# Performance work log

Hardware: AMD Instinct MI355X
Metric: run time of the kernel (lower is better)

Reference implementation:

```python
import jax, jax.numpy as jnp
import numpy as np

B, N, OBS, ACT = 128, 32, 64, 16
D = OBS + ACT       # obs_z_input_dim = 80
H = 64              # hardcoded hidden width
WOUT = 64           # weight_output_dim (d_k_weight)
ZOUT = 64           # obs_z_output_dim (d_k_obsz)
FIN = OBS + ZOUT    # final_input_dim = 128
FOUT = 1            # final_output_dim


def _lin_params(key, fan_in, fan_out):
    k1, k2 = jax.random.split(key)
    w = jax.random.normal(k1, (fan_in, fan_out), jnp.float32) / np.sqrt(fan_in).astype(np.float32)
    b = jax.random.normal(k2, (fan_out,), jnp.float32) * 0.01
    return w, b


def setup_inputs() -> dict:
    key = jax.random.key(0)
    ks = jax.random.split(key, 16)
    inp = {
        "states": jax.random.normal(ks[0], (B, N, OBS), jnp.float32),
        "policies": jax.random.uniform(ks[1], (B, N, ACT), jnp.float32),
        "actions": jax.random.uniform(ks[2], (B, N, ACT), jnp.float32),
    }
    specs = [("kw", OBS, WOUT), ("qw", OBS, WOUT), ("ko", D, ZOUT),
             ("qo", D, ZOUT), ("av", D, ZOUT), ("fv", FIN, FOUT)]
    for idx, (nm, din, dout) in enumerate(specs):
        w1, b1 = _lin_params(ks[3 + 2 * idx], din, H)
        w2, b2 = _lin_params(ks[4 + 2 * idx], H, dout)
        inp[nm + "1_w"], inp[nm + "1_b"] = w1, b1
        inp[nm + "2_w"], inp[nm + "2_b"] = w2, b2
    return inp


def _mlp(x, w1, b1, w2, b2):
    return jax.nn.leaky_relu(x @ w1 + b1) @ w2 + b2


def reference(states, policies, actions,
              kw1_w, kw1_b, kw2_w, kw2_b,
              qw1_w, qw1_b, qw2_w, qw2_b,
              ko1_w, ko1_b, ko2_w, ko2_b,
              qo1_w, qo1_b, qo2_w, qo2_b,
              av1_w, av1_b, av2_w, av2_b,
              fv1_w, fv1_b, fv2_w, fv2_b):
    # --- mixing weight between taken actions and policies ---
    key_z = _mlp(states, kw1_w, kw1_b, kw2_w, kw2_b)    # [B,N,WOUT]
    query_z = _mlp(states, qw1_w, qw1_b, qw2_w, qw2_b)  # [B,N,WOUT]
    # torch: bmm(q, k^T).transpose(1,2) => weight_z[b,a,j] = sigmoid(q[b,j].k[b,a]/sqrt(dk))
    scores_z = jnp.einsum('bad,bjd->baj', key_z, query_z)
    weight_z = jax.nn.sigmoid(scores_z / np.float32(np.sqrt(WOUT)))[..., None]  # [B,N,N,1]

    # z[b,a,j] = w[b,a,j]*actions[b,j] + (1-w)*policies[b,j]
    z = weight_z * actions[:, None, :, :] + (1.0 - weight_z) * policies[:, None, :, :]  # [B,N,N,ACT]
    states_b = jnp.broadcast_to(states[:, None, :, :], (B, N, N, OBS))  # states_rep[b,a,j]=states[b,j]
    obs_z = jnp.concatenate([states_b, z], axis=-1)                     # [B,N,N,D]

    # source_obsz one-hot-diag trick selects obs_z[b,a,a] (broadcast over j)
    diag = jnp.arange(N)
    source = obs_z[:, diag, diag, :]                                    # [B,N,D]
    key_obsz = _mlp(source, ko1_w, ko1_b, ko2_w, ko2_b)                 # [B,N,ZOUT]
    query_obsz = _mlp(obs_z, qo1_w, qo1_b, qo2_w, qo2_b)                # [B,N,N,ZOUT]
    scores_obsz = jnp.sum(key_obsz[:, :, None, :] * query_obsz, axis=-1)  # [B,N,N]
    weight_obsz = jax.nn.softmax(scores_obsz / np.float32(np.sqrt(ZOUT)), axis=-1)
    ret_weight_obsz = weight_obsz[..., None]                            # [B,N,N,1]

    # obs_z_pi[b,a,k,j] = cat(states[b,j], policies[b,j]) if j==k else obs_z[b,a,j]
    # (place_zs / place_policies masking). The attention-value MLP is pointwise
    # over the last dim, so apply it to the two distinct branches and combine:
    vals = _mlp(obs_z, av1_w, av1_b, av2_w, av2_b)                      # [B,N,N,ZOUT]
    sp = jnp.concatenate([states, policies], axis=-1)                   # [B,N,D]
    vals_pi = _mlp(sp, av1_w, av1_b, av2_w, av2_b)                      # [B,N,ZOUT]

    w = weight_obsz  # broadcast weight w5[b,a,k,j] = w[b,a,j]
    sum_all = jnp.einsum('baj,bajd->bad', w, vals)                      # [B,N,ZOUT]
    node_features = (sum_all[:, :, None, :]
                     - w[..., None] * vals
                     + w[..., None] * vals_pi[:, None, :, :]) / N       # [B,N,N,ZOUT]

    node_in = jnp.concatenate([states_b, node_features], axis=-1)       # [B,N,N,FIN]
    value = _mlp(node_in, fv1_w, fv1_b, fv2_w, fv2_b)                   # [B,N,N,1]
    return value, weight_z, ret_weight_obsz
```

## Files before the change

kernel.cpp:

```cpp
#include <hip/hip_runtime.h>

#define NN   32
#define HID  64

typedef __attribute__((ext_vector_type(8))) short bf16x8;
typedef __attribute__((ext_vector_type(4))) float f32x4;
typedef unsigned short u16;
typedef unsigned int   u32;

__device__ __forceinline__ float leaky(float v) { return v >= 0.f ? v : 0.01f * v; }
__device__ __forceinline__ float wsum64(float p) {
#pragma unroll
    for (int o = 32; o; o >>= 1) p += __shfl_xor(p, o);
    return p;
}
__device__ __forceinline__ u16 f2bf(float f) {
    union { float f; u32 u; } v; v.f = f;
    return (u16)((v.u + 0x7FFFu + ((v.u >> 16) & 1)) >> 16);
}
__device__ __forceinline__ bf16x8 pack8(const float* v) {
    bf16x8 r;
#pragma unroll
    for (int e = 0; e < 8; ++e) r[e] = (short)f2bf(v[e]);
    return r;
}
__device__ __forceinline__ int swz(int row, int col)   { return row * 64 + ((((col >> 3) ^ (row & 7)) << 3) | (col & 7)); }
__device__ __forceinline__ int swz32(int row, int col) { return row * 32 + ((((col >> 3) ^ (row & 3)) << 3) | (col & 7)); }

__device__ __forceinline__ f32x4 gemm64(f32x4 C, const u16* A, const u16* W, int lm, int kb8, int bcol) {
#pragma unroll
    for (int k0 = 0; k0 < 64; k0 += 32) {
        const int g = (k0 >> 3) + kb8;
        const bf16x8 a = *(const bf16x8*)&A[lm * 64 + ((g ^ (lm & 7)) << 3)];
        const bf16x8 w = *(const bf16x8*)&W[bcol * 64 + ((g ^ (bcol & 7)) << 3)];
        C = __builtin_amdgcn_mfma_f32_16x16x32_bf16(a, w, C, 0, 0, 0);
    }
    return C;
}
__device__ __forceinline__ f32x4 gemm32(f32x4 C, const u16* A, const u16* W, int lm, int kb8, int bcol) {
    const bf16x8 a = *(const bf16x8*)&A[lm * 32 + ((kb8 ^ (lm & 3)) << 3)];
    const bf16x8 w = *(const bf16x8*)&W[bcol * 32 + ((kb8 ^ (bcol & 3)) << 3)];
    return __builtin_amdgcn_mfma_f32_16x16x32_bf16(a, w, C, 0, 0, 0);
}

#define W_KW1  0
#define W_KW2  4096
#define W_QW1  8192
#define W_QW2  12288
#define W_KO1A 16384
#define W_KO2  20480
#define W_QO2  24576
#define W_QO1A 28672
#define W_AV1A 32768
#define W_FV1A 36864
#define W_KO1B 40960
#define W_QO1B 43008
#define W_AV1B 45056

__global__ __launch_bounds__(256)
void prep_kernel(const float* __restrict__ av2_w, const float* __restrict__ av2_b,
                 const float* __restrict__ fv1_w,
                 const float* __restrict__ kw1_w, const float* __restrict__ kw2_w,
                 const float* __restrict__ qw1_w, const float* __restrict__ qw2_w,
                 const float* __restrict__ ko1_w, const float* __restrict__ ko2_w,
                 const float* __restrict__ qo2_w, const float* __restrict__ qo1_w,
                 const float* __restrict__ av1_w,
                 u16* __restrict__ MT, float* __restrict__ c, u16* __restrict__ wt)
{
    const int blk = blockIdx.x, t = threadIdx.x;
    if (blk == 0) {
        const int h = t & 63, jg = t >> 6;
        __shared__ float sA[4096];
        for (int i = t; i < 4096; i += 256) sA[i] = av2_w[i];
        __syncthreads();
        const float* W = fv1_w + 4096;
        float acc[16];
#pragma unroll
        for (int i = 0; i < 16; ++i) acc[i] = 0.f;
        for (int m = 0; m < 64; ++m) {
            const float w = W[m * 64 + h];
#pragma unroll
            for (int i = 0; i < 16; ++i)
                acc[i] = fmaf(sA[(jg + 4 * i) * 64 + m], w, acc[i]);
        }
#pragma unroll
        for (int i = 0; i < 16; ++i) { const int k = jg + 4 * i; MT[swz(h, k)] = f2bf(acc[i]); }
        if (t < 64) {
            float s = 0.f;
            for (int m = 0; m < 64; ++m) s = fmaf(av2_b[m], W[m * 64 + t], s);
            c[t] = s;
        }
    } else if (blk <= 9) {
        const float* srcs[9] = {kw1_w, kw2_w, qw1_w, qw2_w, ko1_w, ko2_w, qo1_w, av1_w, fv1_w};
        const int    offs[9] = {W_KW1, W_KW2, W_QW1, W_QW2, W_KO1A, W_KO2, W_QO1A, W_AV1A, W_FV1A};
        const float* W = srcs[blk - 1]; u16* dst = wt + offs[blk - 1];
        for (int i = t; i < 4096; i += 256) { const int k = i >> 6, h = i & 63; dst[swz(h, k)] = f2bf(W[i]); }
    } else if (blk == 10) {
        u16* dst = wt + W_QO2;
        for (int i = t; i < 4096; i += 256) { const int h = i >> 6, d = i & 63; dst[swz(h, d)] = f2bf(qo2_w[i]); }
    } else if (blk <= 13) {
        const float* srcs[3] = {ko1_w + 4096, qo1_w + 4096, av1_w + 4096};
        const int    offs[3] = {W_KO1B, W_QO1B, W_AV1B};
        const float* W = srcs[blk - 11]; u16* dst = wt + offs[blk - 11];
        for (int i = t; i < 1024; i += 256) {
            const int k = i >> 6, h = i & 63;
            dst[swz32(h, k)]      = f2bf(W[i]);
            dst[swz32(h, 16 + k)] = 0;
        }
    }
}

__global__ __launch_bounds__(256)
void setup_kernel(const float* __restrict__ states, const float* __restrict__ policies,
                  const float* __restrict__ actions,
                  const float* __restrict__ kw1_b, const float* __restrict__ kw2_b,
                  const float* __restrict__ qw1_b, const float* __restrict__ qw2_b,
                  const float* __restrict__ ko1_b, const float* __restrict__ ko2_b,
                  const float* __restrict__ qo1_b, const float* __restrict__ qo2_b,
                  const float* __restrict__ av1_b, const float* __restrict__ fv1_b,
                  const u16* __restrict__ wt, const u16* __restrict__ MT,
                  const float* __restrict__ c_,
                  u32* __restrict__ kzg, u32* __restrict__ qzg,
                  float* __restrict__ kq, float* __restrict__ kb,
                  float* __restrict__ baseq, float* __restrict__ deltaq,
                  float* __restrict__ basev, float* __restrict__ deltav,
                  float* __restrict__ pre, float* __restrict__ vpf)
{
    const int blk = blockIdx.x;
    const int row0 = blk * 16;
    const int t = threadIdx.x, lane = t & 63, jg = t >> 6;
    const int lm = lane & 15, kb8 = lane >> 4, cg = jg * 16 + lm;

    __shared__ __align__(16) u16 aST[1024], aH1[1024], aH2[1024], aKZ[1024], aQZ[1024];
    __shared__ __align__(16) u16 aP2[512], aDAP[512];
    __shared__ float fACT[256], fPOL[256];
    __shared__ float fKOBS[16 * 68];
    __shared__ float wzd[16];

    {
        const int i = t * 4, row = i >> 6, col = i & 63;
        const float4 s4 = *(const float4*)&states[row0 * 64 + i];
        const int base = swz(row, col);
        aST[base + 0] = f2bf(s4.x); aST[base + 1] = f2bf(s4.y);
        aST[base + 2] = f2bf(s4.z); aST[base + 3] = f2bf(s4.w);
        const float av = actions[row0 * 16 + t], pv = policies[row0 * 16 + t];
        fACT[t] = av; fPOL[t] = pv;
        const int r2 = t >> 4, cc = t & 15;
        aDAP[swz32(r2, cc)]      = f2bf(av - pv);
        aDAP[swz32(r2, 16 + cc)] = 0;
        aP2 [swz32(r2, 16 + cc)] = 0;
    }
    __syncthreads();

    {
        f32x4 C = {0.f,0.f,0.f,0.f};
        C = gemm64(C, aST, wt + W_KW1, lm, kb8, cg);
        const float bv = kw1_b[cg];
#pragma unroll
        for (int rr = 0; rr < 4; ++rr) aH1[swz(kb8 * 4 + rr, cg)] = f2bf(leaky(C[rr] + bv));
    }
    __syncthreads();

    {
        f32x4 C = {0.f,0.f,0.f,0.f};
        C = gemm64(C, aH1, wt + W_KW2, lm, kb8, cg);
        const float bv = kw2_b[cg];
#pragma unroll
        for (int rr = 0; rr < 4; ++rr) aKZ[swz(kb8 * 4 + rr, cg)] = f2bf(C[rr] + bv);
        f32x4 D = {0.f,0.f,0.f,0.f};
        D = gemm64(D, aST, wt + W_QW1, lm, kb8, cg);
        const float bq = qw1_b[cg];
#pragma unroll
        for (int rr = 0; rr < 4; ++rr) aH2[swz(kb8 * 4 + rr, cg)] = f2bf(leaky(D[rr] + bq));
    }
    __syncthreads();

    {
        f32x4 C = {0.f,0.f,0.f,0.f};
        C = gemm64(C, aH2, wt + W_QW2, lm, kb8, cg);
        const float bv = qw2_b[cg];
#pragma unroll
        for (int rr = 0; rr < 4; ++rr) aQZ[swz(kb8 * 4 + rr, cg)] = f2bf(C[rr] + bv);
    }
    __syncthreads();

    if (jg == 0) {
        f32x4 C = {0.f,0.f,0.f,0.f};
#pragma unroll
        for (int k0 = 0; k0 < 64; k0 += 32) {
            const int g = (k0 >> 3) + kb8;
            const bf16x8 a  = *(const bf16x8*)&aKZ[lm * 64 + ((g ^ (lm & 7)) << 3)];
            const bf16x8 qb = *(const bf16x8*)&aQZ[lm * 64 + ((g ^ (lm & 7)) << 3)];
            C = __builtin_amdgcn_mfma_f32_16x16x32_bf16(a, qb, C, 0, 0, 0);
        }
        if ((lm >> 2) == kb8) wzd[lm] = 1.f / (1.f + __expf(-C[lm & 3] * 0.125f));
    } else if (jg == 1) {
        const u32* s = (const u32*)aKZ;
        for (int i = lane; i < 512; i += 64) kzg[blk * 512 + i] = s[i];
    } else if (jg == 2) {
        const u32* s = (const u32*)aQZ;
        for (int i = lane; i < 512; i += 64) qzg[blk * 512 + i] = s[i];
    }
    __syncthreads();

    {
        const int r2 = t >> 4, cc = t & 15;
        const float w = wzd[r2];
        aP2[swz32(r2, cc)] = f2bf(w * fACT[t] + (1.f - w) * fPOL[t]);
    }
    __syncthreads();

    {
        f32x4 C = {0.f,0.f,0.f,0.f};
        C = gemm64(C, aST, wt + W_KO1A, lm, kb8, cg);
        C = gemm32(C, aP2, wt + W_KO1B, lm, kb8, cg);
        const float bv = ko1_b[cg];
#pragma unroll
        for (int rr = 0; rr < 4; ++rr) aH1[swz(kb8 * 4 + rr, cg)] = f2bf(leaky(C[rr] + bv));
    }
    __syncthreads();

    {
        f32x4 C = {0.f,0.f,0.f,0.f};
        C = gemm64(C, aH1, wt + W_KO2, lm, kb8, cg);
        const float bv = ko2_b[cg];
#pragma unroll
        for (int rr = 0; rr < 4; ++rr) {
            const float v = C[rr] + bv;
            aH2[swz(kb8 * 4 + rr, cg)] = f2bf(v);
            fKOBS[(kb8 * 4 + rr) * 68 + cg] = v;
        }
        const int r2 = t >> 4, cc = t & 15;
        aP2[swz32(r2, cc)] = f2bf(fPOL[t]);
    }
    __syncthreads();

    {
        f32x4 C = {0.f,0.f,0.f,0.f};
        C = gemm64(C, aH2, wt + W_QO2, lm, kb8, cg);
#pragma unroll
        for (int rr = 0; rr < 4; ++rr) kq[(row0 + kb8 * 4 + rr) * 64 + cg] = C[rr] * 0.125f;
    }
    {
        const float qb = qo2_b[lane];
#pragma unroll
        for (int q = 0; q < 4; ++q) {
            const int r = jg * 4 + q;
            const float s = wsum64(qb * fKOBS[r * 68 + lane]);
            if (lane == 0) kb[row0 + r] = s * 0.125f;
        }
    }
    {
        f32x4 C = {0.f,0.f,0.f,0.f};
        C = gemm64(C, aST, wt + W_QO1A, lm, kb8, cg);
        C = gemm32(C, aP2, wt + W_QO1B, lm, kb8, cg);
        const float bv = qo1_b[cg];
#pragma unroll
        for (int rr = 0; rr < 4; ++rr) baseq[(row0 + kb8 * 4 + rr) * 64 + cg] = C[rr] + bv;
    }
    {
        f32x4 C = {0.f,0.f,0.f,0.f};
        C = gemm32(C, aDAP, wt + W_QO1B, lm, kb8, cg);
#pragma unroll
        for (int rr = 0; rr < 4; ++rr) deltaq[(row0 + kb8 * 4 + rr) * 64 + cg] = C[rr];
    }
    {
        f32x4 C = {0.f,0.f,0.f,0.f};
        C = gemm64(C, aST, wt + W_AV1A, lm, kb8, cg);
        C = gemm32(C, aP2, wt + W_AV1B, lm, kb8, cg);
        const float bv = av1_b[cg];
#pragma unroll
        for (int rr = 0; rr < 4; ++rr) {
            const float v = C[rr] + bv;
            basev[(row0 + kb8 * 4 + rr) * 64 + cg] = v;
            aH1[swz(kb8 * 4 + rr, cg)] = f2bf(leaky(v));
        }
    }
    {
        f32x4 C = {0.f,0.f,0.f,0.f};
        C = gemm32(C, aDAP, wt + W_AV1B, lm, kb8, cg);
#pragma unroll
        for (int rr = 0; rr < 4; ++rr) deltav[(row0 + kb8 * 4 + rr) * 64 + cg] = C[rr];
    }
    {
        f32x4 C = {0.f,0.f,0.f,0.f};
        C = gemm64(C, aST, wt + W_FV1A, lm, kb8, cg);
        const float bv = fv1_b[cg];
#pragma unroll
        for (int rr = 0; rr < 4; ++rr) pre[(row0 + kb8 * 4 + rr) * 64 + cg] = C[rr] + bv;
    }
    __syncthreads();

    {
        f32x4 C = {0.f,0.f,0.f,0.f};
        C = gemm64(C, aH1, MT, lm, kb8, cg);
        const float bv = c_[cg];
#pragma unroll
        for (int rr = 0; rr < 4; ++rr) vpf[(row0 + kb8 * 4 + rr) * 64 + cg] = C[rr] + bv;
    }
}

__global__ __launch_bounds__(256)
void wz_kernel(const u32* __restrict__ kzg, const u32* __restrict__ qzg,
               float* __restrict__ out_wz)
{
    const int b = blockIdx.x, t = threadIdx.x, lane = t & 63, jg = t >> 6;
    __shared__ __align__(16) u16 sKZ[2048], sQZ[2048];
    u32* kzu = (u32*)sKZ; u32* qzu = (u32*)sQZ;
    for (int i = t; i < 1024; i += 256) { kzu[i] = kzg[b * 1024 + i]; qzu[i] = qzg[b * 1024 + i]; }
    __syncthreads();

    const int lm = lane & 15, kb8 = lane >> 4;
    const int rt = jg >> 1, ct = jg & 1;
    f32x4 acc = {0.f, 0.f, 0.f, 0.f};
#pragma unroll
    for (int k0 = 0; k0 < 64; k0 += 32) {
        const int g = (k0 >> 3) + kb8;
        const int ra = rt * 16 + lm, rb = ct * 16 + lm;
        const bf16x8 af = *(const bf16x8*)&sKZ[ra * 64 + ((g ^ (ra & 7)) << 3)];
        const bf16x8 bf = *(const bf16x8*)&sQZ[rb * 64 + ((g ^ (rb & 7)) << 3)];
        acc = __builtin_amdgcn_mfma_f32_16x16x32_bf16(af, bf, acc, 0, 0, 0);
    }
#pragma unroll
    for (int rr = 0; rr < 4; ++rr) {
        const int arow = rt * 16 + kb8 * 4 + rr;
        const int jcol = ct * 16 + lm;
        out_wz[b * 1024 + arow * 32 + jcol] = 1.f / (1.f + __expf(-acc[rr] * 0.125f));
    }
}

__global__ __launch_bounds__(256)
void main_kernel(const float* __restrict__ wz,
                 const float* __restrict__ kq,    const float* __restrict__ kb,
                 const float* __restrict__ baseq, const float* __restrict__ deltaq,
                 const float* __restrict__ basev, const float* __restrict__ deltav,
                 const float* __restrict__ pre,   const float* __restrict__ vpf,
                 const u16* __restrict__ MT,
                 const float* __restrict__ c,
                 const float* __restrict__ fv2_w, const float* __restrict__ fv2_b,
                 float* __restrict__ out_value,
                 float* __restrict__ out_wobs)
{
    const int bid0 = blockIdx.x;
    const int bid  = (bid0 & 7) * 512 + (bid0 >> 3);
    const int b = bid >> 5, a = bid & 31;
    const int t = threadIdx.x, lane = t & 63, jg = t >> 6;
    const int row = t >> 3, s8 = t & 7, c0 = s8 * 8;

    __shared__ __align__(16) u16 sHV[2048];
    __shared__ float sC[32 * 65];
    __shared__ float sHB[64];
    __shared__ float s_sc[NN];

    const int base = b * 2048 + t * 8;
    const float wzv = wz[b * 1024 + a * 32 + row];
    const float kbv = kb[b * 32 + a];
    const float4 p0 = *(const float4*)&pre[base], p1 = *(const float4*)&pre[base + 4];
    const float4 f0 = *(const float4*)&vpf[base], f1 = *(const float4*)&vpf[base + 4];
    {
        const float4 q0 = *(const float4*)&baseq[base],  q1 = *(const float4*)&baseq[base + 4];
        const float4 d0 = *(const float4*)&deltaq[base], d1 = *(const float4*)&deltaq[base + 4];
        const float4 k0 = *(const float4*)&kq[(b * 32 + a) * 64 + c0];
        const float4 k1 = *(const float4*)&kq[(b * 32 + a) * 64 + c0 + 4];
        float p = leaky(q0.x + wzv * d0.x) * k0.x;
        p = fmaf(leaky(q0.y + wzv * d0.y), k0.y, p);
        p = fmaf(leaky(q0.z + wzv * d0.z), k0.z, p);
        p = fmaf(leaky(q0.w + wzv * d0.w), k0.w, p);
        p = fmaf(leaky(q1.x + wzv * d1.x), k1.x, p);
        p = fmaf(leaky(q1.y + wzv * d1.y), k1.y, p);
        p = fmaf(leaky(q1.z + wzv * d1.z), k1.z, p);
        p = fmaf(leaky(q1.w + wzv * d1.w), k1.w, p);
        p += __shfl_xor(p, 1); p += __shfl_xor(p, 2); p += __shfl_xor(p, 4);
        if (s8 == 0) s_sc[row] = p + kbv;
    }
    {
        const float4 v0 = *(const float4*)&basev[base],  v1 = *(const float4*)&basev[base + 4];
        const float4 e0 = *(const float4*)&deltav[base], e1 = *(const float4*)&deltav[base + 4];
        float hv[8];
        hv[0]=leaky(v0.x+wzv*e0.x); hv[1]=leaky(v0.y+wzv*e0.y); hv[2]=leaky(v0.z+wzv*e0.z); hv[3]=leaky(v0.w+wzv*e0.w);
        hv[4]=leaky(v1.x+wzv*e1.x); hv[5]=leaky(v1.y+wzv*e1.y); hv[6]=leaky(v1.z+wzv*e1.z); hv[7]=leaky(v1.w+wzv*e1.w);
        const int g2 = s8 ^ (row & 7);
        *(bf16x8*)&sHV[row * 64 + (g2 << 3)] = pack8(hv);
    }
    __syncthreads();

    float wreg;
    {
        const float sreg = s_sc[lane & 31];
        float m = sreg;
#pragma unroll
        for (int o = 1; o < 32; o <<= 1) m = fmaxf(m, __shfl_xor(m, o));
        const float e = __expf(sreg - m);
        float ssum = e;
#pragma unroll
        for (int o = 1; o < 32; o <<= 1) ssum += __shfl_xor(ssum, o);
        wreg = e / ssum;
        if (t < 32) out_wobs[b * 1024 + a * 32 + t] = wreg;
    }
    {
        const int lm = lane & 15, kb8 = lane >> 4;
        const int bcol = jg * 16 + lm;
        f32x4 acc0 = {0.f,0.f,0.f,0.f}, acc1 = {0.f,0.f,0.f,0.f};
#pragma unroll
        for (int k0 = 0; k0 < 64; k0 += 32) {
            const int g = (k0 >> 3) + kb8;
            const bf16x8 bf = *(const bf16x8*)&MT[bcol * 64 + (((g ^ (bcol & 7)) << 3))];
            const int r0 = lm, r1 = 16 + lm;
            const bf16x8 a0 = *(const bf16x8*)&sHV[r0 * 64 + (((g ^ (r0 & 7)) << 3))];
            const bf16x8 a1 = *(const bf16x8*)&sHV[r1 * 64 + (((g ^ (r1 & 7)) << 3))];
            acc0 = __builtin_amdgcn_mfma_f32_16x16x32_bf16(a0, bf, acc0, 0, 0, 0);
            acc1 = __builtin_amdgcn_mfma_f32_16x16x32_bf16(a1, bf, acc1, 0, 0, 0);
        }
        float hb = 0.f;
#pragma unroll
        for (int rr = 0; rr < 4; ++rr) {
            const int r0 = kb8 * 4 + rr, r1 = 16 + kb8 * 4 + rr;
            sC[r0 * 65 + bcol] = acc0[rr];
            sC[r1 * 65 + bcol] = acc1[rr];
            hb = fmaf(__shfl(wreg, r0), acc0[rr], hb);
            hb = fmaf(__shfl(wreg, r1), acc1[rr], hb);
        }
        hb += __shfl_xor(hb, 16);
        hb += __shfl_xor(hb, 32);
        if (kb8 == 0 && jg == (bcol >> 4)) sHB[bcol] = hb;
    }
    __syncthreads();

    {
        const float wrow = __shfl(wreg, row);
        const float4 cc0 = *(const float4*)&c[c0],     cc1 = *(const float4*)&c[c0 + 4];
        const float4 fw0 = *(const float4*)&fv2_w[c0], fw1 = *(const float4*)&fv2_w[c0 + 4];
        const float preL[8] = {p0.x,p0.y,p0.z,p0.w,p1.x,p1.y,p1.z,p1.w};
        const float vpfL[8] = {f0.x,f0.y,f0.z,f0.w,f1.x,f1.y,f1.z,f1.w};
        const float cL[8]   = {cc0.x,cc0.y,cc0.z,cc0.w,cc1.x,cc1.y,cc1.z,cc1.w};
        const float fwL[8]  = {fw0.x,fw0.y,fw0.z,fw0.w,fw1.x,fw1.y,fw1.z,fw1.w};
        float vpart = 0.f;
#pragma unroll
        for (int e = 0; e < 8; ++e) {
            const int col = c0 + e;
            float g = preL[e] + (sHB[col] - wrow * sC[row * 65 + col]
                                 + (1.f - wrow) * cL[e] + wrow * vpfL[e]) * (1.f / 32.f);
            g = leaky(g);
            vpart = fmaf(g, fwL[e], vpart);
        }
        vpart += __shfl_xor(vpart, 1); vpart += __shfl_xor(vpart, 2); vpart += __shfl_xor(vpart, 4);
        if (s8 == 0) out_value[b * 1024 + a * 32 + row] = vpart + fv2_b[0];
    }
}

extern "C" void kernel_launch(void* const* d_in, const int* in_sizes, int n_in,
                              void* d_out, int out_size, void* d_ws, size_t ws_size,
                              hipStream_t stream)
{
    const float* states   = (const float*)d_in[0];
    const float* policies = (const float*)d_in[1];
    const float* actions  = (const float*)d_in[2];
    const float* kw1_w = (const float*)d_in[3];  const float* kw1_b = (const float*)d_in[4];
    const float* kw2_w = (const float*)d_in[5];  const float* kw2_b = (const float*)d_in[6];
    const float* qw1_w = (const float*)d_in[7];  const float* qw1_b = (const float*)d_in[8];
    const float* qw2_w = (const float*)d_in[9];  const float* qw2_b = (const float*)d_in[10];
    const float* ko1_w = (const float*)d_in[11]; const float* ko1_b = (const float*)d_in[12];
    const float* ko2_w = (const float*)d_in[13]; const float* ko2_b = (const float*)d_in[14];
    const float* qo1_w = (const float*)d_in[15]; const float* qo1_b = (const float*)d_in[16];
    const float* qo2_w = (const float*)d_in[17]; const float* qo2_b = (const float*)d_in[18];
    const float* av1_w = (const float*)d_in[19]; const float* av1_b = (const float*)d_in[20];
    const float* av2_w = (const float*)d_in[21]; const float* av2_b = (const float*)d_in[22];
    const float* fv1_w = (const float*)d_in[23]; const float* fv1_b = (const float*)d_in[24];
    const float* fv2_w = (const float*)d_in[25]; const float* fv2_b = (const float*)d_in[26];

    float* out       = (float*)d_out;
    float* out_value = out;
    float* out_wz    = out + 131072;
    float* out_wobs  = out + 262144;

    const int SZ = 262144;
    float* ws   = (float*)d_ws;
    float* c_   = ws;
    float* kb_  = ws + 64;
    u16*   MT_  = (u16*)(ws + 4160);
    u32*   kzg  = (u32*)(ws + 6208);
    u32*   qzg  = (u32*)(ws + 137280);
    float* kq_   = ws + 268352;
    float* baseq = kq_   + SZ;
    float* dq_   = baseq + SZ;
    float* basev = dq_   + SZ;
    float* dv_   = basev + SZ;
    float* pre_  = dv_   + SZ;
    float* vpf_  = pre_  + SZ;
    u16*   wt_   = (u16*)(ws + 2103360);

    prep_kernel<<<14, 256, 0, stream>>>(
        av2_w, av2_b, fv1_w,
        kw1_w, kw2_w, qw1_w, qw2_w, ko1_w, ko2_w, qo2_w, qo1_w, av1_w,
        MT_, c_, wt_);

    setup_kernel<<<256, 256, 0, stream>>>(
        states, policies, actions,
        kw1_b, kw2_b, qw1_b, qw2_b, ko1_b, ko2_b, qo1_b, qo2_b, av1_b, fv1_b,
        wt_, MT_, c_,
        kzg, qzg, kq_, kb_, baseq, dq_, basev, dv_, pre_, vpf_);

    wz_kernel<<<128, 256, 0, stream>>>(kzg, qzg, out_wz);

    main_kernel<<<4096, 256, 0, stream>>>(
        out_wz, kq_, kb_, baseq, dq_, basev, dv_, pre_, vpf_,
        MT_, c_, fv2_w, fv2_b,
        out_value, out_wobs);
}
```

Baseline: 40.54 us.

## Fuse wz computation into main kernel and process eight agents per block

```diff
diff --git a/kernel.cpp b/kernel.cpp
--- a/kernel.cpp
+++ b/kernel.cpp
@@ -17,6 +17,10 @@
 __device__ __forceinline__ u16 f2bf(float f) {
     union { float f; u32 u; } v; v.f = f;
     return (u16)((v.u + 0x7FFFu + ((v.u >> 16) & 1)) >> 16);
+}
+__device__ __forceinline__ float bf2f(short s) {
+    union { u32 u; float f; } v; v.u = ((u32)(u16)s) << 16;
+    return v.f;
 }
 __device__ __forceinline__ bf16x8 pack8(const float* v) {
     bf16x8 r;
@@ -301,37 +305,8 @@
 }
 
 __global__ __launch_bounds__(256)
-void wz_kernel(const u32* __restrict__ kzg, const u32* __restrict__ qzg,
-               float* __restrict__ out_wz)
-{
-    const int b = blockIdx.x, t = threadIdx.x, lane = t & 63, jg = t >> 6;
-    __shared__ __align__(16) u16 sKZ[2048], sQZ[2048];
-    u32* kzu = (u32*)sKZ; u32* qzu = (u32*)sQZ;
-    for (int i = t; i < 1024; i += 256) { kzu[i] = kzg[b * 1024 + i]; qzu[i] = qzg[b * 1024 + i]; }
-    __syncthreads();
-
-    const int lm = lane & 15, kb8 = lane >> 4;
-    const int rt = jg >> 1, ct = jg & 1;
-    f32x4 acc = {0.f, 0.f, 0.f, 0.f};
-#pragma unroll
-    for (int k0 = 0; k0 < 64; k0 += 32) {
-        const int g = (k0 >> 3) + kb8;
-        const int ra = rt * 16 + lm, rb = ct * 16 + lm;
-        const bf16x8 af = *(const bf16x8*)&sKZ[ra * 64 + ((g ^ (ra & 7)) << 3)];
-        const bf16x8 bf = *(const bf16x8*)&sQZ[rb * 64 + ((g ^ (rb & 7)) << 3)];
-        acc = __builtin_amdgcn_mfma_f32_16x16x32_bf16(af, bf, acc, 0, 0, 0);
-    }
-#pragma unroll
-    for (int rr = 0; rr < 4; ++rr) {
-        const int arow = rt * 16 + kb8 * 4 + rr;
-        const int jcol = ct * 16 + lm;
-        out_wz[b * 1024 + arow * 32 + jcol] = 1.f / (1.f + __expf(-acc[rr] * 0.125f));
-    }
-}
-
-__global__ __launch_bounds__(256)
-void main_kernel(const float* __restrict__ wz,
-                 const float* __restrict__ kq,    const float* __restrict__ kb,
+void main_kernel(const u32* __restrict__ kzg,   const u32* __restrict__ qzg,
+                 const float* __restrict__ kq,  const float* __restrict__ kb,
                  const float* __restrict__ baseq, const float* __restrict__ deltaq,
                  const float* __restrict__ basev, const float* __restrict__ deltav,
                  const float* __restrict__ pre,   const float* __restrict__ vpf,
@@ -339,112 +314,142 @@
                  const float* __restrict__ c,
                  const float* __restrict__ fv2_w, const float* __restrict__ fv2_b,
                  float* __restrict__ out_value,
+                 float* __restrict__ out_wz,
                  float* __restrict__ out_wobs)
 {
     const int bid0 = blockIdx.x;
-    const int bid  = (bid0 & 7) * 512 + (bid0 >> 3);
-    const int b = bid >> 5, a = bid & 31;
+    const int bid  = (bid0 & 7) * 64 + (bid0 >> 3);
+    const int b = bid >> 2, a0 = (bid & 3) * 8;
     const int t = threadIdx.x, lane = t & 63, jg = t >> 6;
     const int row = t >> 3, s8 = t & 7, c0 = s8 * 8;
 
+    __shared__ __align__(16) u16 sMT[4096];
+    __shared__ __align__(16) u16 sQZ[2048];
+    __shared__ __align__(16) u16 sKZ8[512];
     __shared__ __align__(16) u16 sHV[2048];
+    __shared__ float sKQ[512];
     __shared__ float sC[32 * 65];
     __shared__ float sHB[64];
-    __shared__ float s_sc[NN];
-
-    const int base = b * 2048 + t * 8;
-    const float wzv = wz[b * 1024 + a * 32 + row];
-    const float kbv = kb[b * 32 + a];
-    const float4 p0 = *(const float4*)&pre[base], p1 = *(const float4*)&pre[base + 4];
-    const float4 f0 = *(const float4*)&vpf[base], f1 = *(const float4*)&vpf[base + 4];
-    {
-        const float4 q0 = *(const float4*)&baseq[base],  q1 = *(const float4*)&baseq[base + 4];
-        const float4 d0 = *(const float4*)&deltaq[base], d1 = *(const float4*)&deltaq[base + 4];
-        const float4 k0 = *(const float4*)&kq[(b * 32 + a) * 64 + c0];
-        const float4 k1 = *(const float4*)&kq[(b * 32 + a) * 64 + c0 + 4];
-        float p = leaky(q0.x + wzv * d0.x) * k0.x;
-        p = fmaf(leaky(q0.y + wzv * d0.y), k0.y, p);
-        p = fmaf(leaky(q0.z + wzv * d0.z), k0.z, p);
-        p = fmaf(leaky(q0.w + wzv * d0.w), k0.w, p);
-        p = fmaf(leaky(q1.x + wzv * d1.x), k1.x, p);
-        p = fmaf(leaky(q1.y + wzv * d1.y), k1.y, p);
-        p = fmaf(leaky(q1.z + wzv * d1.z), k1.z, p);
-        p = fmaf(leaky(q1.w + wzv * d1.w), k1.w, p);
-        p += __shfl_xor(p, 1); p += __shfl_xor(p, 2); p += __shfl_xor(p, 4);
-        if (s8 == 0) s_sc[row] = p + kbv;
-    }
-    {
-        const float4 v0 = *(const float4*)&basev[base],  v1 = *(const float4*)&basev[base + 4];
-        const float4 e0 = *(const float4*)&deltav[base], e1 = *(const float4*)&deltav[base + 4];
-        float hv[8];
-        hv[0]=leaky(v0.x+wzv*e0.x); hv[1]=leaky(v0.y+wzv*e0.y); hv[2]=leaky(v0.z+wzv*e0.z); hv[3]=leaky(v0.w+wzv*e0.w);
-        hv[4]=leaky(v1.x+wzv*e1.x); hv[5]=leaky(v1.y+wzv*e1.y); hv[6]=leaky(v1.z+wzv*e1.z); hv[7]=leaky(v1.w+wzv*e1.w);
-        const int g2 = s8 ^ (row & 7);
-        *(bf16x8*)&sHV[row * 64 + (g2 << 3)] = pack8(hv);
-    }
-    __syncthreads();
-
-    float wreg;
-    {
-        const float sreg = s_sc[lane & 31];
-        float m = sreg;
-#pragma unroll
-        for (int o = 1; o < 32; o <<= 1) m = fmaxf(m, __shfl_xor(m, o));
-        const float e = __expf(sreg - m);
-        float ssum = e;
-#pragma unroll
-        for (int o = 1; o < 32; o <<= 1) ssum += __shfl_xor(ssum, o);
-        wreg = e / ssum;
-        if (t < 32) out_wobs[b * 1024 + a * 32 + t] = wreg;
-    }
-    {
-        const int lm = lane & 15, kb8 = lane >> 4;
-        const int bcol = jg * 16 + lm;
-        f32x4 acc0 = {0.f,0.f,0.f,0.f}, acc1 = {0.f,0.f,0.f,0.f};
-#pragma unroll
-        for (int k0 = 0; k0 < 64; k0 += 32) {
-            const int g = (k0 >> 3) + kb8;
-            const bf16x8 bf = *(const bf16x8*)&MT[bcol * 64 + (((g ^ (bcol & 7)) << 3))];
-            const int r0 = lm, r1 = 16 + lm;
-            const bf16x8 a0 = *(const bf16x8*)&sHV[r0 * 64 + (((g ^ (r0 & 7)) << 3))];
-            const bf16x8 a1 = *(const bf16x8*)&sHV[r1 * 64 + (((g ^ (r1 & 7)) << 3))];
-            acc0 = __builtin_amdgcn_mfma_f32_16x16x32_bf16(a0, bf, acc0, 0, 0, 0);
-            acc1 = __builtin_amdgcn_mfma_f32_16x16x32_bf16(a1, bf, acc1, 0, 0, 0);
-        }
-        float hb = 0.f;
-#pragma unroll
-        for (int rr = 0; rr < 4; ++rr) {
-            const int r0 = kb8 * 4 + rr, r1 = 16 + kb8 * 4 + rr;
-            sC[r0 * 65 + bcol] = acc0[rr];
-            sC[r1 * 65 + bcol] = acc1[rr];
-            hb = fmaf(__shfl(wreg, r0), acc0[rr], hb);
-            hb = fmaf(__shfl(wreg, r1), acc1[rr], hb);
-        }
-        hb += __shfl_xor(hb, 16);
-        hb += __shfl_xor(hb, 32);
-        if (kb8 == 0 && jg == (bcol >> 4)) sHB[bcol] = hb;
-    }
-    __syncthreads();
-
-    {
-        const float wrow = __shfl(wreg, row);
-        const float4 cc0 = *(const float4*)&c[c0],     cc1 = *(const float4*)&c[c0 + 4];
-        const float4 fw0 = *(const float4*)&fv2_w[c0], fw1 = *(const float4*)&fv2_w[c0 + 4];
-        const float preL[8] = {p0.x,p0.y,p0.z,p0.w,p1.x,p1.y,p1.z,p1.w};
-        const float vpfL[8] = {f0.x,f0.y,f0.z,f0.w,f1.x,f1.y,f1.z,f1.w};
-        const float cL[8]   = {cc0.x,cc0.y,cc0.z,cc0.w,cc1.x,cc1.y,cc1.z,cc1.w};
-        const float fwL[8]  = {fw0.x,fw0.y,fw0.z,fw0.w,fw1.x,fw1.y,fw1.z,fw1.w};
-        float vpart = 0.f;
-#pragma unroll
-        for (int e = 0; e < 8; ++e) {
-            const int col = c0 + e;
-            float g = preL[e] + (sHB[col] - wrow * sC[row * 65 + col]
-                                 + (1.f - wrow) * cL[e] + wrow * vpfL[e]) * (1.f / 32.f);
-            g = leaky(g);
-            vpart = fmaf(g, fwL[e], vpart);
-        }
-        vpart += __shfl_xor(vpart, 1); vpart += __shfl_xor(vpart, 2); vpart += __shfl_xor(vpart, 4);
-        if (s8 == 0) out_value[b * 1024 + a * 32 + row] = vpart + fv2_b[0];
+    __shared__ float s_sc[32];
+    __shared__ float skb[8];
+
+    {
+        u32* d = (u32*)sMT;  for (int i = t; i < 2048; i += 256) d[i] = ((const u32*)MT)[i];
+        u32* q = (u32*)sQZ;  for (int i = t; i < 1024; i += 256) q[i] = qzg[b * 1024 + i];
+        ((u32*)sKZ8)[t] = kzg[b * 1024 + a0 * 32 + t];
+        for (int i = t; i < 512; i += 256) sKQ[i] = kq[(b * 32 + a0) * 64 + i];
+        if (t < 8) skb[t] = kb[b * 32 + a0 + t];
+    }
+    const int rb = (b * 32 + row) * 64 + c0;
+    const float4 q0 = *(const float4*)&baseq[rb],  q1 = *(const float4*)&baseq[rb + 4];
+    const float4 d0 = *(const float4*)&deltaq[rb], d1 = *(const float4*)&deltaq[rb + 4];
+    const float4 v0 = *(const float4*)&basev[rb],  v1 = *(const float4*)&basev[rb + 4];
+    const float4 e0 = *(const float4*)&deltav[rb], e1 = *(const float4*)&deltav[rb + 4];
+    const float4 p0 = *(const float4*)&pre[rb],    p1 = *(const float4*)&pre[rb + 4];
+    const float4 f0 = *(const float4*)&vpf[rb],    f1 = *(const float4*)&vpf[rb + 4];
+    const float4 cc0 = *(const float4*)&c[c0],     cc1 = *(const float4*)&c[c0 + 4];
+    const float4 fw0 = *(const float4*)&fv2_w[c0], fw1 = *(const float4*)&fv2_w[c0 + 4];
+    const float fb2 = fv2_b[0];
+    const float bqL[8] = {q0.x,q0.y,q0.z,q0.w,q1.x,q1.y,q1.z,q1.w};
+    const float dqL[8] = {d0.x,d0.y,d0.z,d0.w,d1.x,d1.y,d1.z,d1.w};
+    const float bvL[8] = {v0.x,v0.y,v0.z,v0.w,v1.x,v1.y,v1.z,v1.w};
+    const float dvL[8] = {e0.x,e0.y,e0.z,e0.w,e1.x,e1.y,e1.z,e1.w};
+    const float preL[8] = {p0.x,p0.y,p0.z,p0.w,p1.x,p1.y,p1.z,p1.w};
+    const float vpfL[8] = {f0.x,f0.y,f0.z,f0.w,f1.x,f1.y,f1.z,f1.w};
+    const float cL[8]  = {cc0.x,cc0.y,cc0.z,cc0.w,cc1.x,cc1.y,cc1.z,cc1.w};
+    const float fwL[8] = {fw0.x,fw0.y,fw0.z,fw0.w,fw1.x,fw1.y,fw1.z,fw1.w};
+    __syncthreads();
+
+    const int gq = s8 ^ (row & 7);
+
+    for (int ai = 0; ai < 8; ++ai) {
+        const int a = a0 + ai;
+
+        float wzv;
+        {
+            const bf16x8 kzp = *(const bf16x8*)&sKZ8[ai * 64 + ((s8 ^ ai) << 3)];
+            const bf16x8 qzp = *(const bf16x8*)&sQZ[row * 64 + (gq << 3)];
+            float p = 0.f;
+#pragma unroll
+            for (int e = 0; e < 8; ++e)
+                p = fmaf(bf2f(kzp[e]), bf2f(qzp[e]), p);
+            p += __shfl_xor(p, 1); p += __shfl_xor(p, 2); p += __shfl_xor(p, 4);
+            wzv = 1.f / (1.f + __expf(-p * 0.125f));
+            if (s8 == 0) out_wz[b * 1024 + a * 32 + row] = wzv;
+        }
+
+        {
+            float p = 0.f;
+#pragma unroll
+            for (int e = 0; e < 8; ++e)
+                p = fmaf(leaky(bqL[e] + wzv * dqL[e]), sKQ[ai * 64 + c0 + e], p);
+            p += __shfl_xor(p, 1); p += __shfl_xor(p, 2); p += __shfl_xor(p, 4);
+            if (s8 == 0) s_sc[row] = p + skb[ai];
+        }
+
+        {
+            float hv[8];
+#pragma unroll
+            for (int e = 0; e < 8; ++e) hv[e] = leaky(bvL[e] + wzv * dvL[e]);
+            *(bf16x8*)&sHV[row * 64 + (gq << 3)] = pack8(hv);
+        }
+        __syncthreads();
+
+        float wreg;
+        {
+            const float sreg = s_sc[lane & 31];
+            float m = sreg;
+#pragma unroll
+            for (int o = 1; o < 32; o <<= 1) m = fmaxf(m, __shfl_xor(m, o));
+            const float e = __expf(sreg - m);
+            float ssum = e;
+#pragma unroll
+            for (int o = 1; o < 32; o <<= 1) ssum += __shfl_xor(ssum, o);
+            wreg = e / ssum;
+            if (t < 32) out_wobs[b * 1024 + a * 32 + t] = wreg;
+        }
+
+        {
+            const int lm = lane & 15, kb8 = lane >> 4;
+            const int bcol = jg * 16 + lm;
+            f32x4 acc0 = {0.f,0.f,0.f,0.f}, acc1 = {0.f,0.f,0.f,0.f};
+#pragma unroll
+            for (int k0 = 0; k0 < 64; k0 += 32) {
+                const int g = (k0 >> 3) + kb8;
+                const bf16x8 bf = *(const bf16x8*)&sMT[bcol * 64 + ((g ^ (bcol & 7)) << 3)];
+                const bf16x8 A0 = *(const bf16x8*)&sHV[lm * 64 + ((g ^ (lm & 7)) << 3)];
+                const bf16x8 A1 = *(const bf16x8*)&sHV[(16 + lm) * 64 + ((g ^ (lm & 7)) << 3)];
+                acc0 = __builtin_amdgcn_mfma_f32_16x16x32_bf16(A0, bf, acc0, 0, 0, 0);
+                acc1 = __builtin_amdgcn_mfma_f32_16x16x32_bf16(A1, bf, acc1, 0, 0, 0);
+            }
+            float hb = 0.f;
+#pragma unroll
+            for (int rr = 0; rr < 4; ++rr) {
+                const int r0 = kb8 * 4 + rr, r1 = 16 + r0;
+                sC[r0 * 65 + bcol] = acc0[rr];
+                sC[r1 * 65 + bcol] = acc1[rr];
+                hb = fmaf(__shfl(wreg, r0), acc0[rr], hb);
+                hb = fmaf(__shfl(wreg, r1), acc1[rr], hb);
+            }
+            hb += __shfl_xor(hb, 16);
+            hb += __shfl_xor(hb, 32);
+            if (lane < 16) sHB[bcol] = hb;
+        }
+        __syncthreads();
+
+        {
+            const float wrow = __shfl(wreg, row);
+            float vpart = 0.f;
+#pragma unroll
+            for (int e = 0; e < 8; ++e) {
+                const int col = c0 + e;
+                float g = preL[e] + (sHB[col] - wrow * sC[row * 65 + col]
+                                     + (1.f - wrow) * cL[e] + wrow * vpfL[e]) * (1.f / 32.f);
+                vpart = fmaf(leaky(g), fwL[e], vpart);
+            }
+            vpart += __shfl_xor(vpart, 1); vpart += __shfl_xor(vpart, 2); vpart += __shfl_xor(vpart, 4);
+            if (s8 == 0) out_value[b * 1024 + a * 32 + row] = vpart + fb2;
+        }
     }
 }
 
@@ -500,10 +505,8 @@
         wt_, MT_, c_,
         kzg, qzg, kq_, kb_, baseq, dq_, basev, dv_, pre_, vpf_);
 
-    wz_kernel<<<128, 256, 0, stream>>>(kzg, qzg, out_wz);
-
-    main_kernel<<<4096, 256, 0, stream>>>(
-        out_wz, kq_, kb_, baseq, dq_, basev, dv_, pre_, vpf_,
+    main_kernel<<<512, 256, 0, stream>>>(
+        kzg, qzg, kq_, kb_, baseq, dq_, basev, dv_, pre_, vpf_,
         MT_, c_, fv2_w, fv2_b,
-        out_value, out_wobs);
-}
+        out_value, out_wz, out_wobs);
+}
```

Measured after the change: 44.56 us. 9.9% more time.

## Fuse sigmoid weight computation into main kernel and drop wz_kernel launch

Applied to the files above, without the earlier changes.

```diff
diff --git a/kernel.cpp b/kernel.cpp
--- a/kernel.cpp
+++ b/kernel.cpp
@@ -17,6 +17,10 @@
 __device__ __forceinline__ u16 f2bf(float f) {
     union { float f; u32 u; } v; v.f = f;
     return (u16)((v.u + 0x7FFFu + ((v.u >> 16) & 1)) >> 16);
+}
+__device__ __forceinline__ float bf2f(short s) {
+    union { u32 u; float f; } v; v.u = ((u32)(u16)s) << 16;
+    return v.f;
 }
 __device__ __forceinline__ bf16x8 pack8(const float* v) {
     bf16x8 r;
@@ -301,37 +305,8 @@
 }
 
 __global__ __launch_bounds__(256)
-void wz_kernel(const u32* __restrict__ kzg, const u32* __restrict__ qzg,
-               float* __restrict__ out_wz)
-{
-    const int b = blockIdx.x, t = threadIdx.x, lane = t & 63, jg = t >> 6;
-    __shared__ __align__(16) u16 sKZ[2048], sQZ[2048];
-    u32* kzu = (u32*)sKZ; u32* qzu = (u32*)sQZ;
-    for (int i = t; i < 1024; i += 256) { kzu[i] = kzg[b * 1024 + i]; qzu[i] = qzg[b * 1024 + i]; }
-    __syncthreads();
-
-    const int lm = lane & 15, kb8 = lane >> 4;
-    const int rt = jg >> 1, ct = jg & 1;
-    f32x4 acc = {0.f, 0.f, 0.f, 0.f};
-#pragma unroll
-    for (int k0 = 0; k0 < 64; k0 += 32) {
-        const int g = (k0 >> 3) + kb8;
-        const int ra = rt * 16 + lm, rb = ct * 16 + lm;
-        const bf16x8 af = *(const bf16x8*)&sKZ[ra * 64 + ((g ^ (ra & 7)) << 3)];
-        const bf16x8 bf = *(const bf16x8*)&sQZ[rb * 64 + ((g ^ (rb & 7)) << 3)];
-        acc = __builtin_amdgcn_mfma_f32_16x16x32_bf16(af, bf, acc, 0, 0, 0);
-    }
-#pragma unroll
-    for (int rr = 0; rr < 4; ++rr) {
-        const int arow = rt * 16 + kb8 * 4 + rr;
-        const int jcol = ct * 16 + lm;
-        out_wz[b * 1024 + arow * 32 + jcol] = 1.f / (1.f + __expf(-acc[rr] * 0.125f));
-    }
-}
-
-__global__ __launch_bounds__(256)
-void main_kernel(const float* __restrict__ wz,
-                 const float* __restrict__ kq,    const float* __restrict__ kb,
+void main_kernel(const u32* __restrict__ kzg,   const u32* __restrict__ qzg,
+                 const float* __restrict__ kq,  const float* __restrict__ kb,
                  const float* __restrict__ baseq, const float* __restrict__ deltaq,
                  const float* __restrict__ basev, const float* __restrict__ deltav,
                  const float* __restrict__ pre,   const float* __restrict__ vpf,
@@ -339,6 +314,7 @@
                  const float* __restrict__ c,
                  const float* __restrict__ fv2_w, const float* __restrict__ fv2_b,
                  float* __restrict__ out_value,
+                 float* __restrict__ out_wz,
                  float* __restrict__ out_wobs)
 {
     const int bid0 = blockIdx.x;
@@ -350,13 +326,30 @@
     __shared__ __align__(16) u16 sHV[2048];
     __shared__ float sC[32 * 65];
     __shared__ float sHB[64];
-    __shared__ float s_sc[NN];
+    __shared__ float s_sc[32];
 
     const int base = b * 2048 + t * 8;
-    const float wzv = wz[b * 1024 + a * 32 + row];
     const float kbv = kb[b * 32 + a];
     const float4 p0 = *(const float4*)&pre[base], p1 = *(const float4*)&pre[base + 4];
     const float4 f0 = *(const float4*)&vpf[base], f1 = *(const float4*)&vpf[base + 4];
+
+    float wzv;
+    {
+        const int Ga = s8 ^ (a & 7);
+        const u32* kzt = kzg + ((b * 2 + (a >> 4)) << 9) + ((a & 15) << 5) + (Ga << 2);
+        const int Gj = s8 ^ (row & 7);
+        const u32* qzt = qzg + ((b * 2 + (row >> 4)) << 9) + ((row & 15) << 5) + (Gj << 2);
+        float p = 0.f;
+#pragma unroll
+        for (int e = 0; e < 4; ++e) {
+            const u32 ku = kzt[e], qu = qzt[e];
+            p = fmaf(bf2f((short)(ku & 0xFFFF)), bf2f((short)(qu & 0xFFFF)), p);
+            p = fmaf(bf2f((short)(ku >> 16)),   bf2f((short)(qu >> 16)),   p);
+        }
+        p += __shfl_xor(p, 1); p += __shfl_xor(p, 2); p += __shfl_xor(p, 4);
+        wzv = 1.f / (1.f + __expf(-p * 0.125f));
+        if (s8 == 0) out_wz[b * 1024 + a * 32 + row] = wzv;
+    }
     {
         const float4 q0 = *(const float4*)&baseq[base],  q1 = *(const float4*)&baseq[base + 4];
         const float4 d0 = *(const float4*)&deltaq[base], d1 = *(const float4*)&deltaq[base + 4];
@@ -422,7 +415,7 @@
         }
         hb += __shfl_xor(hb, 16);
         hb += __shfl_xor(hb, 32);
-        if (kb8 == 0 && jg == (bcol >> 4)) sHB[bcol] = hb;
+        if (lane < 16) sHB[bcol] = hb;
     }
     __syncthreads();
 
@@ -500,10 +493,8 @@
         wt_, MT_, c_,
         kzg, qzg, kq_, kb_, baseq, dq_, basev, dv_, pre_, vpf_);
 
-    wz_kernel<<<128, 256, 0, stream>>>(kzg, qzg, out_wz);
-
     main_kernel<<<4096, 256, 0, stream>>>(
-        out_wz, kq_, kb_, baseq, dq_, basev, dv_, pre_, vpf_,
+        kzg, qzg, kq_, kb_, baseq, dq_, basev, dv_, pre_, vpf_,
         MT_, c_, fv2_w, fv2_b,
-        out_value, out_wobs);
-}
+        out_value, out_wz, out_wobs);
+}
```

New measurement: 39.46 us. -2.7%, faster.
